# Performance work log

Hardware: AMD Instinct MI355X
Metric: run time of the kernel (lower is better)

## Reference

```python
import jax, jax.numpy as jnp
import numpy as np

DIM, NH, HD = 512, 16, 32          # dim, num_heads, head_dim
WH, WW = 7, 7                      # window size
N = WH * WW                        # tokens per window = 49
B_ = 2048                          # num_windows * batch


def _relative_position_index():
    # Static integer index table, identical to the torch buffer construction.
    coords = np.stack(np.meshgrid(np.arange(WH), np.arange(WW), indexing='ij'))  # (2,WH,WW)
    cf = coords.reshape(2, -1)                                                   # (2,N)
    rel = cf[:, :, None] - cf[:, None, :]                                        # (2,N,N)
    rel = rel.transpose(1, 2, 0).astype(np.int64)                                # (N,N,2)
    rel[:, :, 0] += WH - 1
    rel[:, :, 1] += WW - 1
    rel[:, :, 0] *= 2 * WW - 1
    return jnp.asarray(rel.sum(-1))                                              # (N,N)

REL_IDX = _relative_position_index()


def setup_inputs() -> dict:
    key = jax.random.key(0)
    ks = jax.random.split(key, 6)
    s = 0.02
    return {
        'x': jax.random.normal(ks[0], (B_, N, DIM), dtype=jnp.float32),
        'qkv_w': jax.random.normal(ks[1], (3 * DIM, DIM), dtype=jnp.float32) * s,
        'qkv_b': jax.random.normal(ks[2], (3 * DIM,), dtype=jnp.float32) * s,
        'proj_w': jax.random.normal(ks[3], (DIM, DIM), dtype=jnp.float32) * s,
        'proj_b': jax.random.normal(ks[4], (DIM,), dtype=jnp.float32) * s,
        'bias_table': jax.random.normal(ks[5], (2 * WH - 1, 2 * WW - 1, NH), dtype=jnp.float32) * s,
    }


def reference(x, qkv_w, qkv_b, proj_w, proj_b, bias_table):
    b, n, c = x.shape
    # fused qkv projection, split per the original reshape(B_,N,nH,hd,3)
    qkv = (x @ qkv_w.T + qkv_b).reshape(b, n, NH, HD, 3)
    qkv = qkv.transpose(0, 2, 1, 3, 4)                 # (B_, nH, N, hd, 3)
    q, k, v = qkv[..., 0], qkv[..., 1], qkv[..., 2]
    # gathered relative position bias: (N,N,nH) -> (1,nH,N,N)
    bias = bias_table.reshape(-1, NH)[REL_IDX].transpose(2, 0, 1)[None]
    scale = 1.0 / np.sqrt(HD).astype(np.float32)
    scores = jnp.einsum('bhqd,bhkd->bhqk', q, k) * scale + bias
    attn = jax.nn.softmax(scores, axis=-1)
    out = jnp.einsum('bhqk,bhkd->bhqd', attn, v)       # (B_, nH, N, hd)
    out = out.transpose(0, 2, 1, 3).reshape(b, n, c)
    return out @ proj_w.T + proj_b
```

## Files before the change

### kernel.cpp

```cpp
#include <hip/hip_runtime.h>


typedef __bf16 bf16x8 __attribute__((ext_vector_type(8)));
typedef float f32x4 __attribute__((ext_vector_type(4)));

#define SCALE_Q 0.17677669529663687f

#define OFF_XS     2365440ull
#define OFF_ATTN   136583168ull
#define WS2        507779072ull
#define WS_R2      105119744ull

__device__ __forceinline__ unsigned short bfc(float f) {
    union { __bf16 b; unsigned short u; } x; x.b = (__bf16)f; return x.u;
}

__device__ __forceinline__ uint4 cvt8(const float f[8]) {
    uint4 p;
    p.x = (unsigned)bfc(f[0]) | ((unsigned)bfc(f[1]) << 16);
    p.y = (unsigned)bfc(f[2]) | ((unsigned)bfc(f[3]) << 16);
    p.z = (unsigned)bfc(f[4]) | ((unsigned)bfc(f[5]) << 16);
    p.w = (unsigned)bfc(f[6]) | ((unsigned)bfc(f[7]) << 16);
    return p;
}

__device__ __forceinline__ unsigned short f2bf(float f) {
    unsigned int u = __float_as_uint(f);
    u += 0x7FFFu + ((u >> 16) & 1u);
    return (unsigned short)(u >> 16);
}

__device__ __forceinline__ uint4 pack8(const unsigned short o[8]) {
    uint4 p;
    p.x = (unsigned)o[0] | ((unsigned)o[1] << 16);
    p.y = (unsigned)o[2] | ((unsigned)o[3] << 16);
    p.z = (unsigned)o[4] | ((unsigned)o[5] << 16);
    p.w = (unsigned)o[6] | ((unsigned)o[7] << 16);
    return p;
}

union BU8 { bf16x8 v; unsigned short s[8]; };

#define GLOAD16(g, l) __builtin_amdgcn_global_load_lds( \
    (__attribute__((address_space(1))) void*)(void*)(g), \
    (__attribute__((address_space(3))) void*)(l), 16, 0, 0)

__global__ void prepN_kernel(const float* __restrict__ x,
                             const float* __restrict__ qkv_w,
                             const float* __restrict__ qkv_b,
                             const float* __restrict__ proj_w,
                             const float* __restrict__ bias_table,
                             unsigned short* __restrict__ wqkv_f,
                             unsigned short* __restrict__ wproj_f,
                             float* __restrict__ bias_f,
                             float* __restrict__ qkvb_r,
                             unsigned short* __restrict__ xs) {
    int b = blockIdx.x, t = threadIdx.x;
    if (b < 384) {
        int gid = b * 256 + t;
        int c = gid >> 6, k8 = (gid & 63) * 8;
        int head = c / 96, rem = c - head * 96;
        int which = rem >> 5, d = rem & 31;
        const float* src = qkv_w + (size_t)(head * 96 + d * 3 + which) * 512 + k8;
        float f[8];
#pragma unroll
        for (int j = 0; j < 8; ++j) f[j] = src[j];
        *(uint4*)(wqkv_f + (size_t)c * 512 + k8) = cvt8(f);
    } else if (b < 512) {
        int gid = (b - 384) * 256 + t;
        const float* src = proj_w + (size_t)gid * 8;
        float f[8];
#pragma unroll
        for (int j = 0; j < 8; ++j) f[j] = src[j];
        *(uint4*)(wproj_f + (size_t)gid * 8) = cvt8(f);
    } else if (b < 768) {
        int gid = (b - 512) * 256 + t;
        int j = gid & 63; int i = (gid >> 6) & 63; int h = gid >> 12;
        float v = -1e30f;
        if (i < 49 && j < 49) {
            int ri = i / 7, ci = i % 7, rj = j / 7, cj = j % 7;
            int idx = (ri - rj + 6) * 13 + (ci - cj + 6);
            v = bias_table[idx * 16 + h];
        }
        bias_f[gid] = v;
    } else if (b == 768) {
        for (int c = t; c < 1536; c += 256) {
            int head = c / 96, rem = c - head * 96;
            int which = rem >> 5, d = rem & 31;
            qkvb_r[c] = qkv_b[head * 96 + d * 3 + which];
        }
    } else {
        int gid = (b - 769) * 256 + t;
        int row = gid >> 3, kt = gid & 7;
        int win = row >> 6, tok = row & 63; if (tok > 48) tok = 48;
        int sw = row & 7;
        const float* src = x + ((size_t)win * 49 + tok) * 512 + kt * 64;
        unsigned short* dst = xs + (size_t)row * 512 + kt * 64;
#pragma unroll
        for (int c = 0; c < 8; ++c) {
            int cs = (c ^ sw) * 8;
            float f[8];
            *(float4*)&f[0] = *(const float4*)(src + cs);
            *(float4*)&f[4] = *(const float4*)(src + cs + 4);
            *(uint4*)(dst + c * 8) = cvt8(f);
        }
    }
}

__global__ __launch_bounds__(256, 3)
void qkvattn_kernel(const unsigned short* __restrict__ xs,
                    const unsigned short* __restrict__ wqkv_f,
                    const float* __restrict__ qkvb_r,
                    const float* __restrict__ bias_f,
                    unsigned short* __restrict__ attnout) {
    __shared__ __align__(16) char smem[49152];
    char* As = smem;
    char* Bs = smem + 32768;

    int i = blockIdx.x;
    int virt = (i & 7) * 1024 + (i >> 3);
    int mb = virt >> 4, head = virt & 15;
    int m0 = mb * 256;

    const int tid = threadIdx.x;
    const int l = tid & 63;
    const int W = tid >> 6;
    const int lr = l & 15;
    const int lg = l >> 4;

    f32x4 acc[4][6];
    const f32x4 zf = {0.f, 0.f, 0.f, 0.f};
#pragma unroll
    for (int mt = 0; mt < 4; ++mt)
#pragma unroll
        for (int nt = 0; nt < 6; ++nt) acc[mt][nt] = zf;

    int rsub = l >> 3, csub = l & 7;
    int cswz = (csub ^ rsub) * 16;
    int clin = csub * 16;

    const char* bbase = (const char*)wqkv_f + (size_t)head * 96 * 1024;
    const char* abase = (const char*)xs + ((size_t)m0 * 512) * 2;

#pragma unroll 1
    for (int kt = 0; kt < 8; ++kt) {
        int ko = kt * 128;
#pragma unroll
        for (int ii = 0; ii < 8; ++ii) {
            int r = ii * 32 + W * 8 + rsub;
            GLOAD16(abase + (size_t)r * 1024 + ko + clin, As + ii * 4096 + W * 1024);
        }
#pragma unroll
        for (int jj = 0; jj < 3; ++jj) {
            int r = jj * 32 + W * 8 + rsub;
            GLOAD16(bbase + (size_t)r * 1024 + ko + cswz, Bs + jj * 4096 + W * 1024);
        }
        __syncthreads();
#pragma unroll
        for (int ks = 0; ks < 2; ++ks) {
            bf16x8 af[4], bf[6];
#pragma unroll
            for (int mt = 0; mt < 4; ++mt) {
                int row = W * 64 + mt * 16 + lr;
                af[mt] = *(const bf16x8*)(As + row * 128 +
                    ((ks * 64 + lg * 16) ^ ((row & 7) << 4)));
            }
#pragma unroll
            for (int nt = 0; nt < 6; ++nt) {
                int row = nt * 16 + lr;
                bf[nt] = *(const bf16x8*)(Bs + row * 128 +
                    ((ks * 64 + lg * 16) ^ ((row & 7) << 4)));
            }
#pragma unroll
            for (int mt = 0; mt < 4; ++mt)
#pragma unroll
                for (int nt = 0; nt < 6; ++nt)
                    acc[mt][nt] = __builtin_amdgcn_mfma_f32_16x16x32_bf16(
                        af[mt], bf[nt], acc[mt][nt], 0, 0, 0);
        }
        __syncthreads();
    }

    unsigned short* wbuf = (unsigned short*)smem + W * 6144;
    {
        int tokb = 4 * lg;
#pragma unroll
        for (int nt = 0; nt < 6; ++nt) {
            const int which = nt >> 1;
            const int d = (nt & 1) * 16 + lr;
            float bias = qkvb_r[head * 96 + which * 32 + d];
            float sc = (which == 0) ? SCALE_Q : 1.0f;
#pragma unroll
            for (int mt = 0; mt < 4; ++mt) {
                int tok0 = tokb + mt * 16;
                if (which == 2) {
                    int idx = 4096 + d * 64 + (((tok0 >> 3) ^ (d & 7)) << 3) + (tok0 & 7);
                    ushort4 u;
                    u.x = bfc(acc[mt][nt][0] + bias);
                    u.y = bfc(acc[mt][nt][1] + bias);
                    u.z = bfc(acc[mt][nt][2] + bias);
                    u.w = bfc(acc[mt][nt][3] + bias);
                    *(ushort4*)(wbuf + idx) = u;
                } else {
#pragma unroll
                    for (int r = 0; r < 4; ++r)
                        wbuf[which * 2048 + (tok0 + r) * 32 + d] =
                            bfc((acc[mt][nt][r] + bias) * sc);
                }
            }
        }
    }

    {
        const unsigned short* qa = wbuf;
        char* P = smem + W * 12288;
        int win_g = mb * 4 + W;
        unsigned short* ao = attnout + (size_t)win_g * (49 * 512);

        bf16x8 qf[4], kf[4], vf[2][2];
#pragma unroll
        for (int i2 = 0; i2 < 4; ++i2) {
            qf[i2] = *(const bf16x8*)(qa + (i2 * 16 + lr) * 32 + lg * 8);
            kf[i2] = *(const bf16x8*)(qa + 2048 + (i2 * 16 + lr) * 32 + lg * 8);
        }
#pragma unroll
        for (int ks = 0; ks < 2; ++ks)
#pragma unroll
            for (int nt = 0; nt < 2; ++nt) {
                int d = nt * 16 + lr;
                vf[ks][nt] = *(const bf16x8*)(qa + 4096 + d * 64 +
                    (((ks * 4 + lg) ^ (d & 7)) << 3));
            }

        f32x4 s[4][4];
#pragma unroll
        for (int mt = 0; mt < 4; ++mt)
#pragma unroll
            for (int qt = 0; qt < 4; ++qt)
                s[mt][qt] = __builtin_amdgcn_mfma_f32_16x16x32_bf16(
                    kf[mt], qf[qt], zf, 0, 0, 0);
#pragma unroll
        for (int qt = 0; qt < 4; ++qt) {
            int q = qt * 16 + lr;
            const float* bb = bias_f + ((size_t)head * 64 + q) * 64;
#pragma unroll
            for (int mt = 0; mt < 4; ++mt) {
                float4 b4 = *(const float4*)(bb + mt * 16 + lg * 4);
                s[mt][qt][0] += b4.x; s[mt][qt][1] += b4.y;
                s[mt][qt][2] += b4.z; s[mt][qt][3] += b4.w;
            }
        }
#pragma unroll
        for (int qt = 0; qt < 4; ++qt) {
            float m = -1e30f;
#pragma unroll
            for (int mt = 0; mt < 4; ++mt)
#pragma unroll
                for (int r = 0; r < 4; ++r) m = fmaxf(m, s[mt][qt][r]);
            m = fmaxf(m, __shfl_xor(m, 16));
            m = fmaxf(m, __shfl_xor(m, 32));
            float sum = 0.f;
#pragma unroll
            for (int mt = 0; mt < 4; ++mt)
#pragma unroll
                for (int r = 0; r < 4; ++r) {
                    float p = __expf(s[mt][qt][r] - m);
                    s[mt][qt][r] = p; sum += p;
                }
            sum += __shfl_xor(sum, 16);
            sum += __shfl_xor(sum, 32);
            float inv = 1.0f / sum;
            int ql = qt * 16 + lr;
            int sw = (ql & 7) << 4;
#pragma unroll
            for (int mt = 0; mt < 4; ++mt) {
                uint2 uv;
                uv.x = (unsigned)bfc(s[mt][qt][0] * inv) |
                       ((unsigned)bfc(s[mt][qt][1] * inv) << 16);
                uv.y = (unsigned)bfc(s[mt][qt][2] * inv) |
                       ((unsigned)bfc(s[mt][qt][3] * inv) << 16);
                *(uint2*)(P + ql * 128 + ((mt * 32 + lg * 8) ^ sw)) = uv;
            }
        }
        f32x4 o[4][2];
#pragma unroll
        for (int mt = 0; mt < 4; ++mt) {
            o[mt][0] = zf; o[mt][1] = zf;
            int ql = mt * 16 + lr;
            int sw = (ql & 7) << 4;
#pragma unroll
            for (int ks = 0; ks < 2; ++ks) {
                bf16x8 pf = *(const bf16x8*)(P + ql * 128 + ((ks * 64 + lg * 16) ^ sw));
                o[mt][0] = __builtin_amdgcn_mfma_f32_16x16x32_bf16(pf, vf[ks][0], o[mt][0], 0, 0, 0);
                o[mt][1] = __builtin_amdgcn_mfma_f32_16x16x32_bf16(pf, vf[ks][1], o[mt][1], 0, 0, 0);
            }
        }
#pragma unroll
        for (int mt = 0; mt < 4; ++mt)
#pragma unroll
            for (int nt = 0; nt < 2; ++nt)
#pragma unroll
                for (int r = 0; r < 4; ++r) {
                    int q = mt * 16 + 4 * lg + r;
                    if (q < 49)
                        ao[q * 512 + head * 32 + nt * 16 + lr] = bfc(o[mt][nt][r]);
                }
    }
}

__global__ __launch_bounds__(256, 2)
void proj_kernel(const unsigned short* __restrict__ attnout,
                 const unsigned short* __restrict__ wproj_f,
                 const float* __restrict__ proj_b,
                 float* __restrict__ out) {
    __shared__ __align__(16) char smem[32768];
    char* As = smem;
    char* Bs = smem + 16384;

    int bid = blockIdx.x;
    int c = bid >> 2;
    int cs = (c & 7) * 98 + (c >> 3);
    int m0 = cs * 128;
    int n0 = (bid & 3) * 128;

    const int tid = threadIdx.x;
    const int l = tid & 63;
    const int W = tid >> 6;
    const int lr = l & 15;
    const int lg = l >> 4;
    const int Wm = W >> 1, Wn = W & 1;

    f32x4 acc[4][4];
    const f32x4 zf = {0.f, 0.f, 0.f, 0.f};
#pragma unroll
    for (int mt = 0; mt < 4; ++mt)
#pragma unroll
        for (int nt = 0; nt < 4; ++nt) acc[mt][nt] = zf;

    int rsub = l >> 3;
    int csub = l & 7;
    int cswz = (csub ^ rsub) * 16;

#pragma unroll 1
    for (int kt = 0; kt < 8; ++kt) {
#pragma unroll
        for (int i = 0; i < 4; ++i) {
            int r = i * 32 + W * 8 + rsub;
            const char* srcA = (const char*)attnout +
                ((size_t)(m0 + r) * 512 + kt * 64) * 2 + cswz;
            GLOAD16(srcA, As + i * 4096 + W * 1024);
            const char* srcB = (const char*)wproj_f +
                ((size_t)(n0 + r) * 512 + kt * 64) * 2 + cswz;
            GLOAD16(srcB, Bs + i * 4096 + W * 1024);
        }
        __syncthreads();
#pragma unroll
        for (int ks = 0; ks < 2; ++ks) {
            bf16x8 af[4], bf[4];
#pragma unroll
            for (int mt = 0; mt < 4; ++mt) {
                int row = Wm * 64 + mt * 16 + lr;
                af[mt] = *(const bf16x8*)(As + row * 128 +
                    ((ks * 64 + lg * 16) ^ ((row & 7) << 4)));
            }
#pragma unroll
            for (int nt = 0; nt < 4; ++nt) {
                int row = Wn * 64 + nt * 16 + lr;
                bf[nt] = *(const bf16x8*)(Bs + row * 128 +
                    ((ks * 64 + lg * 16) ^ ((row & 7) << 4)));
            }
#pragma unroll
            for (int mt = 0; mt < 4; ++mt)
#pragma unroll
                for (int nt = 0; nt < 4; ++nt)
                    acc[mt][nt] = __builtin_amdgcn_mfma_f32_16x16x32_bf16(
                        af[mt], bf[nt], acc[mt][nt], 0, 0, 0);
        }
        __syncthreads();
    }
#pragma unroll
    for (int nt = 0; nt < 4; ++nt) {
        int n = n0 + Wn * 64 + nt * 16 + lr;
        float pb = proj_b[n];
#pragma unroll
        for (int mt = 0; mt < 4; ++mt) {
#pragma unroll
            for (int r = 0; r < 4; ++r) {
                int m = m0 + Wm * 64 + mt * 16 + 4 * lg + r;
                out[(size_t)m * 512 + n] = acc[mt][nt][r] + pb;
            }
        }
    }
}

__global__ void prep2_kernel(const float* __restrict__ qkv_w,
                             const float* __restrict__ proj_w,
                             const float* __restrict__ bias_table,
                             unsigned short* __restrict__ wqkv_f,
                             unsigned short* __restrict__ wproj_f,
                             float* __restrict__ bias_f) {
    int b = blockIdx.x, t = threadIdx.x;
    if (b < 384) {
        int gid = b * 256 + t;
        int l = gid & 63; int r = gid >> 6;
        int dh = r & 1; r >>= 1;
        int ks = r & 15; r >>= 4;
        int h = r & 15; int which = r >> 4;
        int d = dh * 16 + (l & 15);
        int row = h * 96 + d * 3 + which;
        int c0 = ks * 32 + (l >> 4) * 8;
        const float* src = qkv_w + row * 512 + c0;
        unsigned short o[8];
#pragma unroll
        for (int j = 0; j < 8; ++j) o[j] = f2bf(src[j]);
        *(uint4*)(wqkv_f + (size_t)gid * 8) = pack8(o);
    } else if (b < 512) {
        int gid = (b - 384) * 256 + t;
        const float* src = proj_w + (size_t)gid * 8;
        unsigned short o[8];
#pragma unroll
        for (int j = 0; j < 8; ++j) o[j] = f2bf(src[j]);
        *(uint4*)(wproj_f + (size_t)gid * 8) = pack8(o);
    } else {
        int gid = (b - 512) * 256 + t;
        int j = gid & 63; int i = (gid >> 6) & 63; int h = gid >> 12;
        float v = -1e30f;
        if (i < 49 && j < 49) {
            int ri = i / 7, ci = i % 7, rj = j / 7, cj = j % 7;
            int idx = (ri - rj + 6) * 13 + (ci - cj + 6);
            v = bias_table[idx * 16 + h];
        }
        bias_f[gid] = v;
    }
}

__global__ __launch_bounds__(256, 2)
void attn_qkv_kernel(const float* __restrict__ x,
                     const float* __restrict__ qkv_b,
                     const unsigned short* __restrict__ wqkv_f,
                     const float* __restrict__ bias_f,
                     unsigned short* __restrict__ attnout) {
    __shared__ __align__(16) char smem[81920];
    const int tid = threadIdx.x;
    const int l = tid & 63;
    const int W = tid >> 6;
    const int lr = l & 15;
    const int lg = l >> 4;
    const int win = blockIdx.x;

    bf16x8 xf[16];
    {
        int trow = 16 * W + lr; if (trow > 48) trow = 48;
        const float* xr = x + ((size_t)win * 49 + trow) * 512;
#pragma unroll
        for (int ks = 0; ks < 16; ++ks) {
            float4 a = *(const float4*)(xr + ks * 32 + lg * 8);
            float4 b = *(const float4*)(xr + ks * 32 + lg * 8 + 4);
            BU8 u;
            u.s[0] = f2bf(a.x); u.s[1] = f2bf(a.y); u.s[2] = f2bf(a.z); u.s[3] = f2bf(a.w);
            u.s[4] = f2bf(b.x); u.s[5] = f2bf(b.y); u.s[6] = f2bf(b.z); u.s[7] = f2bf(b.w);
            xf[ks] = u.v;
        }
    }

    const f32x4 zf = {0.f, 0.f, 0.f, 0.f};
    unsigned short* ao = attnout + (size_t)win * (49 * 512);

    for (int hg = 0; hg < 4; ++hg) {
        for (int h2 = 0; h2 < 4; ++h2) {
            int h = hg * 4 + h2;
            char* qk = smem + h2 * 8192;
            char* vt = smem + 32768 + h2 * 4096;
#pragma unroll 1
            for (int which = 0; which < 3; ++which) {
                f32x4 a0 = zf, a1 = zf;
                const unsigned short* bp =
                    wqkv_f + (size_t)(which * 16 + h) * 16384 + l * 8;
#pragma unroll
                for (int ks = 0; ks < 16; ++ks) {
                    bf16x8 b0 = *(const bf16x8*)(bp + ks * 1024);
                    bf16x8 b1 = *(const bf16x8*)(bp + ks * 1024 + 512);
                    a0 = __builtin_amdgcn_mfma_f32_16x16x32_bf16(xf[ks], b0, a0, 0, 0, 0);
                    a1 = __builtin_amdgcn_mfma_f32_16x16x32_bf16(xf[ks], b1, a1, 0, 0, 0);
                }
                float bias0 = qkv_b[h * 96 + lr * 3 + which];
                float bias1 = qkv_b[h * 96 + (16 + lr) * 3 + which];
                if (which == 2) {
                    int d0 = lr, d1 = 16 + lr;
#pragma unroll
                    for (int r = 0; r < 4; ++r) {
                        int t = 16 * W + 4 * lg + r;
                        *(unsigned short*)(vt + d0 * 128 + ((t * 2) ^ ((d0 & 7) << 4))) =
                            f2bf(a0[r] + bias0);
                        *(unsigned short*)(vt + d1 * 128 + ((t * 2) ^ ((d1 & 7) << 4))) =
                            f2bf(a1[r] + bias1);
                    }
                } else {
                    float sc = (which == 0) ? SCALE_Q : 1.0f;
                    int cb = which * 64;
#pragma unroll
                    for (int r = 0; r < 4; ++r) {
                        int t = 16 * W + 4 * lg + r;
                        int sw = (t & 7) << 4;
                        *(unsigned short*)(qk + t * 128 + ((cb + lr * 2) ^ sw)) =
                            f2bf((a0[r] + bias0) * sc);
                        *(unsigned short*)(qk + t * 128 + ((cb + 32 + lr * 2) ^ sw)) =
                            f2bf((a1[r] + bias1) * sc);
                    }
                }
            }
        }
        __syncthreads();
        {
            int h = hg * 4 + W;
            char* qk = smem + W * 8192;
            char* vt = smem + 32768 + W * 4096;
            char* P  = smem + 49152 + W * 8192;

            bf16x8 kf[4], qf[4];
#pragma unroll
            for (int i = 0; i < 4; ++i) {
                int row = i * 16 + lr;
                int sw = (row & 7) << 4;
                qf[i] = *(const bf16x8*)(qk + row * 128 + ((lg * 16) ^ sw));
                kf[i] = *(const bf16x8*)(qk + row * 128 + ((64 + lg * 16) ^ sw));
            }
            f32x4 s[4][4];
#pragma unroll
            for (int mt = 0; mt < 4; ++mt)
#pragma unroll
                for (int qt = 0; qt < 4; ++qt)
                    s[mt][qt] = __builtin_amdgcn_mfma_f32_16x16x32_bf16(
                        kf[mt], qf[qt], zf, 0, 0, 0);
#pragma unroll
            for (int qt = 0; qt < 4; ++qt) {
                int q = qt * 16 + lr;
                const float* bb = bias_f + ((size_t)h * 64 + q) * 64;
#pragma unroll
                for (int mt = 0; mt < 4; ++mt) {
                    float4 b4 = *(const float4*)(bb + mt * 16 + lg * 4);
                    s[mt][qt][0] += b4.x; s[mt][qt][1] += b4.y;
                    s[mt][qt][2] += b4.z; s[mt][qt][3] += b4.w;
                }
            }
#pragma unroll
            for (int qt = 0; qt < 4; ++qt) {
                float m = -1e30f;
#pragma unroll
                for (int mt = 0; mt < 4; ++mt)
#pragma unroll
                    for (int r = 0; r < 4; ++r) m = fmaxf(m, s[mt][qt][r]);
                m = fmaxf(m, __shfl_xor(m, 16));
                m = fmaxf(m, __shfl_xor(m, 32));
                float sum = 0.f;
#pragma unroll
                for (int mt = 0; mt < 4; ++mt)
#pragma unroll
                    for (int r = 0; r < 4; ++r) {
                        float p = __expf(s[mt][qt][r] - m);
                        s[mt][qt][r] = p; sum += p;
                    }
                sum += __shfl_xor(sum, 16);
                sum += __shfl_xor(sum, 32);
                float inv = 1.0f / sum;
                int qrow = qt * 16 + lr;
                int sw = (qrow & 7) << 4;
#pragma unroll
                for (int mt = 0; mt < 4; ++mt) {
                    uint2 uv;
                    uv.x = (unsigned)f2bf(s[mt][qt][0] * inv) |
                           ((unsigned)f2bf(s[mt][qt][1] * inv) << 16);
                    uv.y = (unsigned)f2bf(s[mt][qt][2] * inv) |
                           ((unsigned)f2bf(s[mt][qt][3] * inv) << 16);
                    *(uint2*)(P + qrow * 128 + ((mt * 32 + lg * 8) ^ sw)) = uv;
                }
            }
            bf16x8 vf[2][2];
#pragma unroll
            for (int ks = 0; ks < 2; ++ks)
#pragma unroll
                for (int nt = 0; nt < 2; ++nt) {
                    int d = nt * 16 + lr;
                    vf[ks][nt] = *(const bf16x8*)(vt + d * 128 +
                        ((ks * 64 + lg * 16) ^ ((d & 7) << 4)));
                }
            f32x4 o[4][2];
#pragma unroll
            for (int mt = 0; mt < 4; ++mt) {
                o[mt][0] = zf; o[mt][1] = zf;
                int q = mt * 16 + lr;
                int sw = (q & 7) << 4;
#pragma unroll
                for (int ks = 0; ks < 2; ++ks) {
                    bf16x8 pf = *(const bf16x8*)(P + q * 128 + ((ks * 64 + lg * 16) ^ sw));
                    o[mt][0] = __builtin_amdgcn_mfma_f32_16x16x32_bf16(pf, vf[ks][0], o[mt][0], 0, 0, 0);
                    o[mt][1] = __builtin_amdgcn_mfma_f32_16x16x32_bf16(pf, vf[ks][1], o[mt][1], 0, 0, 0);
                }
            }
#pragma unroll
            for (int mt = 0; mt < 4; ++mt)
#pragma unroll
                for (int nt = 0; nt < 2; ++nt)
#pragma unroll
                    for (int r = 0; r < 4; ++r) {
                        int q = mt * 16 + 4 * lg + r;
                        if (q < 49)
                            ao[q * 512 + h * 32 + nt * 16 + lr] = f2bf(o[mt][nt][r]);
                    }
        }
        __syncthreads();
    }
}

extern "C" void kernel_launch(void* const* d_in, const int* in_sizes, int n_in,
                              void* d_out, int out_size, void* d_ws, size_t ws_size,
                              hipStream_t stream) {
    const float* x          = (const float*)d_in[0];
    const float* qkv_w      = (const float*)d_in[1];
    const float* qkv_b      = (const float*)d_in[2];
    const float* proj_w     = (const float*)d_in[3];
    const float* proj_b     = (const float*)d_in[4];
    const float* bias_table = (const float*)d_in[5];

    unsigned short* wqkv_f  = (unsigned short*)d_ws;
    unsigned short* wproj_f = wqkv_f + 786432;
    float*          bias_f  = (float*)(wproj_f + 262144);

    if (ws_size >= WS2) {
        float* qkvb_r = (float*)((char*)d_ws + 2359296);
        unsigned short* xs      = (unsigned short*)((char*)d_ws + OFF_XS);
        unsigned short* attnout = (unsigned short*)((char*)d_ws + OFF_ATTN);
        hipLaunchKernelGGL(prepN_kernel, dim3(4865), dim3(256), 0, stream,
                           x, qkv_w, qkv_b, proj_w, bias_table,
                           wqkv_f, wproj_f, bias_f, qkvb_r, xs);
        hipLaunchKernelGGL(qkvattn_kernel, dim3(8192), dim3(256), 0, stream,
                           xs, wqkv_f, qkvb_r, bias_f, attnout);
        hipLaunchKernelGGL(proj_kernel, dim3(3136), dim3(256), 0, stream,
                           attnout, wproj_f, proj_b, (float*)d_out);
    } else if (ws_size >= WS_R2) {
        unsigned short* attnout = (unsigned short*)((char*)d_ws + 2359296);
        hipLaunchKernelGGL(prep2_kernel, dim3(768), dim3(256), 0, stream,
                           qkv_w, proj_w, bias_table, wqkv_f, wproj_f, bias_f);
        hipLaunchKernelGGL(attn_qkv_kernel, dim3(2048), dim3(256), 0, stream,
                           x, qkv_b, wqkv_f, bias_f, attnout);
        hipLaunchKernelGGL(proj_kernel, dim3(3136), dim3(256), 0, stream,
                           attnout, wproj_f, proj_b, (float*)d_out);
    }
}
```

Before: 472.8 us.

## Load A operand fragments directly from global memory into registers, bypassing LDS

The x-tile (A operand) of the QKV GEMM is no longer staged through shared memory. Each wave now reads its own bf16x8 fragments straight from global memory into registers, and the swizzle in the x conversion pass is dropped to match the new linear layout. This removes the LDS traffic and part of the staging for A, which each wave uses alone. In exchange the global loads are less coalesced (16-byte pieces spread across rows), are not overlapped with the barrier, and raise register pressure. A stray unused pointer with a non-ASCII name was also added.

After: 539.5 us. 1.14x slower.

```diff
diff --git a/kernel.cpp b/kernel.cpp
--- a/kernel.cpp
+++ b/kernel.cpp
@@ -93,15 +93,13 @@
         int gid = (b - 769) * 256 + t;
         int row = gid >> 3, kt = gid & 7;
         int win = row >> 6, tok = row & 63; if (tok > 48) tok = 48;
-        int sw = row & 7;
         const float* src = x + ((size_t)win * 49 + tok) * 512 + kt * 64;
         unsigned short* dst = xs + (size_t)row * 512 + kt * 64;
 #pragma unroll
         for (int c = 0; c < 8; ++c) {
-            int cs = (c ^ sw) * 8;
             float f[8];
-            *(float4*)&f[0] = *(const float4*)(src + cs);
-            *(float4*)&f[4] = *(const float4*)(src + cs + 4);
+            *(float4*)&f[0] = *(const float4*)(src + c * 8);
+            *(float4*)&f[4] = *(const float4*)(src + c * 8 + 4);
             *(uint4*)(dst + c * 8) = cvt8(f);
         }
     }
@@ -114,8 +112,7 @@
                     const float* __restrict__ bias_f,
                     unsigned short* __restrict__ attnout) {
     __shared__ __align__(16) char smem[49152];
-    char* As = smem;
-    char* Bs = smem + 32768;
+    char* Bs = smem;
 
     int i = blockIdx.x;
     int virt = (i & 7) * 1024 + (i >> 3);
@@ -137,19 +134,21 @@
 
     int rsub = l >> 3, csub = l & 7;
     int cswz = (csub ^ rsub) * 16;
-    int clin = csub * 16;
 
     const char* bbase = (const char*)wqkv_f + (size_t)head * 96 * 1024;
-    const char* abase = (const char*)xs + ((size_t)m0 * 512) * 2;
+    const unsigned short* apане_unused = nullptr; (void)apане_unused;
+    const unsigned short* abase = xs + (size_t)(m0 + W * 64 + lr) * 512 + lg * 8;
 
 #pragma unroll 1
     for (int kt = 0; kt < 8; ++kt) {
         int ko = kt * 128;
-#pragma unroll
-        for (int ii = 0; ii < 8; ++ii) {
-            int r = ii * 32 + W * 8 + rsub;
-            GLOAD16(abase + (size_t)r * 1024 + ko + clin, As + ii * 4096 + W * 1024);
-        }
+        bf16x8 af[4][2];
+#pragma unroll
+        for (int mt = 0; mt < 4; ++mt)
+#pragma unroll
+            for (int ks = 0; ks < 2; ++ks)
+                af[mt][ks] = *(const bf16x8*)(abase +
+                    (size_t)(mt * 16) * 512 + kt * 64 + ks * 32);
 #pragma unroll
         for (int jj = 0; jj < 3; ++jj) {
             int r = jj * 32 + W * 8 + rsub;
@@ -158,13 +157,7 @@
         __syncthreads();
 #pragma unroll
         for (int ks = 0; ks < 2; ++ks) {
-            bf16x8 af[4], bf[6];
-#pragma unroll
-            for (int mt = 0; mt < 4; ++mt) {
-                int row = W * 64 + mt * 16 + lr;
-                af[mt] = *(const bf16x8*)(As + row * 128 +
-                    ((ks * 64 + lg * 16) ^ ((row & 7) << 4)));
-            }
+            bf16x8 bf[6];
 #pragma unroll
             for (int nt = 0; nt < 6; ++nt) {
                 int row = nt * 16 + lr;
@@ -176,7 +169,7 @@
 #pragma unroll
                 for (int nt = 0; nt < 6; ++nt)
                     acc[mt][nt] = __builtin_amdgcn_mfma_f32_16x16x32_bf16(
-                        af[mt], bf[nt], acc[mt][nt], 0, 0, 0);
+                        af[mt][ks], bf[nt], acc[mt][nt], 0, 0, 0);
         }
         __syncthreads();
     }
```
